# Kernel tuning notes

Hardware: AMD Instinct MI355X
Metric: run time of the kernel (lower is better)

The kernel has to match this reference:

```python
import jax, jax.numpy as jnp
import numpy as np

VOCAB, E, H, HOPS, HEADS = 32000, 128, 256, 3, 4
N, TM, WLEN, TQ = 32, 50, 20, 20


def _gru(x_tbe, h0, Wih, Whh, bih, bhh):
    # x_tbe: [T, B, E] time-major; h0: [B, H]. PyTorch GRU gate order (r, z, n).
    def step(h, xt):
        gi = xt @ Wih.T + bih
        gh = h @ Whh.T + bhh
        ir, iz, inn = jnp.split(gi, 3, axis=-1)
        hr, hz, hn = jnp.split(gh, 3, axis=-1)
        r = jax.nn.sigmoid(ir + hr)
        z = jax.nn.sigmoid(iz + hz)
        n = jnp.tanh(inn + r * hn)
        return (1.0 - z) * n + z * h, None
    h, _ = jax.lax.scan(step, h0, x_tbe)
    return h


def setup_inputs() -> dict:
    key = jax.random.key(0)
    ks = jax.random.split(key, 24)
    f32 = jnp.float32
    emb = jax.random.uniform(ks[0], (VOCAB, E), f32, -3 ** 0.5, 3 ** 0.5)
    emb = emb.at[0].set(0.0)  # padding_idx=0
    s = 0.05
    inp = {
        'stories': jax.random.randint(ks[1], (N, TM, WLEN), 0, VOCAB),
        'questions': jax.random.randint(ks[2], (N, TQ), 0, VOCAB),
        'emb': emb,
        'q_Wih': jax.random.normal(ks[3], (3 * H, E), f32) * s,
        'q_Whh': jax.random.normal(ks[4], (3 * H, H), f32) * s,
        'q_bih': jnp.zeros((3 * H,), f32),
        'q_bhh': jnp.zeros((3 * H,), f32),
        'i_Wih': jax.random.normal(ks[5], (3 * H, E), f32) * s,
        'i_Whh': jax.random.normal(ks[6], (3 * H, H), f32) * s,
        'i_bih': jnp.zeros((3 * H,), f32),
        'i_bhh': jnp.zeros((3 * H,), f32),
        'Wm': jax.random.normal(ks[7], (HOPS, HEADS, H, H), f32) * s,
        'Wo_w': jax.random.normal(ks[8], (HOPS, H, HEADS * H), f32) * s,
        'Wo_b': jnp.full((HOPS, H), 0.01, f32),
        'ft_W1': jax.random.normal(ks[9], (H, H), f32) * s,
        'ft_b1': jnp.full((H,), 0.01, f32),
        'ft_W2': jax.random.normal(ks[10], (H, H), f32) * s,
        'ft_b2': jnp.full((H,), 0.01, f32),
        'g_W1': jax.random.normal(ks[11], (3 * H, 3 * H), f32) * s,
        'g_b1': jnp.full((3 * H,), 0.01, f32),
        'g_W2': jax.random.normal(ks[12], (3 * H, 3 * H), f32) * s,
        'g_b2': jnp.full((3 * H,), 0.01, f32),
        'V_w': jax.random.normal(ks[13], (VOCAB, 3 * H), f32) * s,
    }
    return inp


def reference(stories, questions, emb, q_Wih, q_Whh, q_bih, q_bhh,
              i_Wih, i_Whh, i_bih, i_bhh, Wm, Wo_w, Wo_b,
              ft_W1, ft_b1, ft_W2, ft_b2, g_W1, g_b1, g_W2, g_b2, V_w):
    n, tm, _ = stories.shape
    h = i_Whh.shape[1]
    hops, heads = Wm.shape[0], Wm.shape[1]

    # ---- input module: per-batch-item GRU; hidden state carries across batch items (as in source loop) ----
    story_embs = emb[stories]  # [N, TM, W, E]
    def bstep(hid, se):  # se: [TM, W, E]
        hid2 = _gru(jnp.swapaxes(se, 0, 1), hid, i_Wih, i_Whh, i_bih, i_bhh)
        return hid2, hid2
    _, memory = jax.lax.scan(bstep, jnp.zeros((tm, h), emb.dtype), story_embs)  # [N, TM, H]

    # ---- question module ----
    q_emb = emb[questions]  # [N, TQ, E]
    q = _gru(jnp.swapaxes(q_emb, 0, 1), jnp.zeros((n, h), emb.dtype), q_Wih, q_Whh, q_bih, q_bhh)  # [N, H]

    def ft(x):
        return jax.nn.relu(jax.nn.relu(x @ ft_W1.T + ft_b1) @ ft_W2.T + ft_b2)

    # ---- multi-hop attention controllers ----
    o_k = ft(q)
    buffers = []
    for hp in range(hops):
        proj = jnp.tanh(jnp.einsum('ntd,hed->nhte', memory, Wm[hp]))      # [N,heads,TM,H]
        scores = jax.nn.softmax(jnp.einsum('nhte,ne->nht', proj, o_k), axis=-1)
        rep = jnp.einsum('nht,ntd->nhd', scores, memory)                   # [N,heads,H]
        buf = rep.reshape(n, heads * h) @ Wo_w[hp].T + Wo_b[hp]            # [N,H]
        buffers.append(buf)
        o_k = ft(buf)
    wb = jnp.stack(buffers, axis=1)  # [N, HOPS, H]

    # ---- RM: all-pairs relation MLP (dropout = identity in eval) ----
    npair = hops * hops
    left = jnp.broadcast_to(wb[:, None, :, :], (n, hops, hops, h)).reshape(n, npair, h)
    right = jnp.broadcast_to(wb[:, :, None, :], (n, hops, hops, h)).reshape(n, npair, h)
    qx = jnp.broadcast_to(q[:, None, :], (n, npair, h))
    comb = jnp.concatenate([left, right, qx], axis=-1)                     # [N, HOPS^2, 3H]
    g = jax.nn.relu(jax.nn.relu(comb @ g_W1.T + g_b1) @ g_W2.T + g_b2)
    reasoning = g.sum(axis=1)                                              # [N, 3H]
    return reasoning @ V_w.T                                               # [N, VOCAB]
```

## Files before the change

kernel.cpp:

```cpp
#include <hip/hip_runtime.h>
#include <cmath>

#define VOCABN 32000
#define EE 128
#define HH 256
#define H3 768
#define HOPSN 3
#define HEADSN 4
#define NB 32
#define TMN 50
#define WLENN 20
#define TQN 20
#define NPOS (NB*TMN*WLENN)
#define NQPOS (NB*TQN)

#define OFF_MEM    0
#define OFF_Q      (OFF_MEM + NB*TMN*HH)
#define OFF_OK     (OFF_Q + NB*HH)
#define OFF_WB     (OFF_OK + NB*HH)
#define OFF_REP    (OFF_WB + NB*HOPSN*HH)
#define OFF_REAS   (OFF_REP + NB*HEADSN*HH)
#define OFF_Y1     (OFF_REAS + NB*H3)
#define OFF_PROJ   (OFF_Y1 + NB*9*H3)
#define OFF_EMBP   OFF_PROJ
#define OFF_GI     (OFF_PROJ + NB*12*TMN*HH)

typedef __fp16 h2 __attribute__((ext_vector_type(2)));

__device__ __forceinline__ float sigm(float x) { return 1.f / (1.f + expf(-x)); }

__device__ __forceinline__ unsigned packh2(float x, float y) {
    h2 h = __builtin_amdgcn_cvt_pkrtz(x, y);
    return __builtin_bit_cast(unsigned, h);
}

__device__ __forceinline__ float fdot2u(unsigned a, unsigned b, float c) {
    return __builtin_amdgcn_fdot2(__builtin_bit_cast(h2, a),
                                  __builtin_bit_cast(h2, b), c, false);
}

#define LW(v, base, i8) { const float4 A_ = reinterpret_cast<const float4*>(base)[2*(i8)];     \
                          const float4 B_ = reinterpret_cast<const float4*>(base)[2*(i8)+1];   \
                          v.x = packh2(A_.x, A_.y); v.y = packh2(A_.z, A_.w);                  \
                          v.z = packh2(B_.x, B_.y); v.w = packh2(B_.z, B_.w); }

__global__ __launch_bounds__(256) void k_pack(const float* __restrict__ emb, float* __restrict__ ws)
{
    unsigned* __restrict__ embp = (unsigned*)(ws + OFF_EMBP);
    const int idx = blockIdx.x * 256 + threadIdx.x;
    if (idx < VOCABN * (EE / 2)) {
        const float2 e2 = reinterpret_cast<const float2*>(emb)[idx];
        embp[idx] = packh2(e2.x, e2.y);
    }
}

#define GIB 64
__global__ __launch_bounds__(768) void k_gi2(const int* __restrict__ stories,
                                             const int* __restrict__ questions,
                                             const float* __restrict__ iWih,
                                             const float* __restrict__ qWih,
                                             const float* __restrict__ ibih, const float* __restrict__ ibhh,
                                             const float* __restrict__ qbih, const float* __restrict__ qbhh,
                                             float* __restrict__ ws)
{
    __fp16* __restrict__ gi = (__fp16*)(ws + OFF_GI);
    const unsigned* __restrict__ embp = (const unsigned*)(ws + OFF_EMBP);
    const int j = threadIdx.x;
    const bool isq = blockIdx.x >= (NPOS / GIB);
    const int pblk = isq ? (blockIdx.x - NPOS / GIB) : blockIdx.x;
    const int p0 = pblk * GIB;
    const size_t g0 = (isq ? (size_t)NPOS : 0) + (size_t)p0;
    const int* __restrict__ toks = isq ? (questions + p0) : (stories + p0);
    const float* __restrict__ Wih = isq ? qWih : iWih;
    const float* __restrict__ bih = isq ? qbih : ibih;
    const float* __restrict__ bhh = isq ? qbhh : ibhh;
    const float bias = (j < 2 * HH) ? (bih[j] + bhh[j]) : bih[j];
    const float* wrowp = Wih + (size_t)j * EE;
    uint4 v_0, v_1, v_2, v_3, v_4, v_5, v_6, v_7, v_8, v_9, v_10, v_11, v_12, v_13, v_14, v_15;
    LW(v_0, wrowp, 0)  LW(v_1, wrowp, 1)  LW(v_2, wrowp, 2)  LW(v_3, wrowp, 3)
    LW(v_4, wrowp, 4)  LW(v_5, wrowp, 5)  LW(v_6, wrowp, 6)  LW(v_7, wrowp, 7)
    LW(v_8, wrowp, 8)  LW(v_9, wrowp, 9)  LW(v_10, wrowp, 10) LW(v_11, wrowp, 11)
    LW(v_12, wrowp, 12) LW(v_13, wrowp, 13) LW(v_14, wrowp, 14) LW(v_15, wrowp, 15)

#define DOTG(i) { const uint4 xv = xg[i];                                     \
    acc = fdot2u(xv.x, v_##i.x, acc); acc = fdot2u(xv.y, v_##i.y, acc);       \
    acc = fdot2u(xv.z, v_##i.z, acc); acc = fdot2u(xv.w, v_##i.w, acc); }

    for (int p = 0; p < GIB; ++p) {
        const int tok = toks[p];
        const uint4* __restrict__ xg =
            reinterpret_cast<const uint4*>(embp + (size_t)tok * (EE / 2));
        float acc = bias;
        DOTG(0)  DOTG(1)  DOTG(2)  DOTG(3)  DOTG(4)  DOTG(5)  DOTG(6)  DOTG(7)
        DOTG(8)  DOTG(9)  DOTG(10) DOTG(11) DOTG(12) DOTG(13) DOTG(14) DOTG(15)
        gi[(g0 + p) * H3 + j] = (__fp16)acc;
    }
#undef DOTG
}

__global__ __attribute__((amdgpu_flat_work_group_size(512, 512), amdgpu_waves_per_eu(2, 2)))
void k_gru7(
    const float* __restrict__ iWhh, const float* __restrict__ qWhh,
    const float* __restrict__ ibhh, const float* __restrict__ qbhh,
    float* __restrict__ ws)
{
    __shared__ unsigned hp32[HH / 2];
    __shared__ float red[HH * 5];
    const int tid = threadIdx.x;
    const int j = tid & 255, kh = tid >> 8;
    const int blk = blockIdx.x;
    const bool isq = blk >= TMN;
    const float* __restrict__ Whh = isq ? qWhh : iWhh;
    const float* row0 = Whh + (size_t)j * HH + kh * 128;
    const float* row1 = Whh + (size_t)(HH + j) * HH + kh * 128;
    const float* row2 = Whh + (size_t)(2 * HH + j) * HH + kh * 128;
    uint4 w0_0, w0_1, w0_2, w0_3, w0_4, w0_5, w0_6, w0_7,
          w0_8, w0_9, w0_10, w0_11, w0_12, w0_13, w0_14, w0_15;
    uint4 w1_0, w1_1, w1_2, w1_3, w1_4, w1_5, w1_6, w1_7,
          w1_8, w1_9, w1_10, w1_11, w1_12, w1_13, w1_14, w1_15;
    uint4 w2_0, w2_1, w2_2, w2_3, w2_4, w2_5, w2_6, w2_7,
          w2_8, w2_9, w2_10, w2_11, w2_12, w2_13, w2_14, w2_15;
    LW(w0_0, row0, 0)  LW(w0_1, row0, 1)  LW(w0_2, row0, 2)  LW(w0_3, row0, 3)
    LW(w0_4, row0, 4)  LW(w0_5, row0, 5)  LW(w0_6, row0, 6)  LW(w0_7, row0, 7)
    LW(w0_8, row0, 8)  LW(w0_9, row0, 9)  LW(w0_10, row0, 10) LW(w0_11, row0, 11)
    LW(w0_12, row0, 12) LW(w0_13, row0, 13) LW(w0_14, row0, 14) LW(w0_15, row0, 15)
    LW(w1_0, row1, 0)  LW(w1_1, row1, 1)  LW(w1_2, row1, 2)  LW(w1_3, row1, 3)
    LW(w1_4, row1, 4)  LW(w1_5, row1, 5)  LW(w1_6, row1, 6)  LW(w1_7, row1, 7)
    LW(w1_8, row1, 8)  LW(w1_9, row1, 9)  LW(w1_10, row1, 10) LW(w1_11, row1, 11)
    LW(w1_12, row1, 12) LW(w1_13, row1, 13) LW(w1_14, row1, 14) LW(w1_15, row1, 15)
    LW(w2_0, row2, 0)  LW(w2_1, row2, 1)  LW(w2_2, row2, 2)  LW(w2_3, row2, 3)
    LW(w2_4, row2, 4)  LW(w2_5, row2, 5)  LW(w2_6, row2, 6)  LW(w2_7, row2, 7)
    LW(w2_8, row2, 8)  LW(w2_9, row2, 9)  LW(w2_10, row2, 10) LW(w2_11, row2, 11)
    LW(w2_12, row2, 12) LW(w2_13, row2, 13) LW(w2_14, row2, 14) LW(w2_15, row2, 15)

    float bnH = 0.f, hstate = 0.f;
    if (kh == 0) bnH = (isq ? qbhh : ibhh)[2 * HH + j];
    if (tid < HH / 2) hp32[tid] = 0u;
    const __fp16* __restrict__ gib = (const __fp16*)(ws + OFF_GI)
                                     + (isq ? (size_t)NPOS * H3 : 0);
    float* __restrict__ memv = ws + OFF_MEM;
    float* __restrict__ qv   = ws + OFF_Q;
    __syncthreads();

#define DOT(i) { const uint4 hv = hp4[kh * 16 + (i)];                        \
    a0 = fdot2u(hv.x, w0_##i.x, a0); a0 = fdot2u(hv.y, w0_##i.y, a0);        \
    a0 = fdot2u(hv.z, w0_##i.z, a0); a0 = fdot2u(hv.w, w0_##i.w, a0);        \
    a1 = fdot2u(hv.x, w1_##i.x, a1); a1 = fdot2u(hv.y, w1_##i.y, a1);        \
    a1 = fdot2u(hv.z, w1_##i.z, a1); a1 = fdot2u(hv.w, w1_##i.w, a1);        \
    a2 = fdot2u(hv.x, w2_##i.x, a2); a2 = fdot2u(hv.y, w2_##i.y, a2);        \
    a2 = fdot2u(hv.z, w2_##i.z, a2); a2 = fdot2u(hv.w, w2_##i.w, a2); }

    const int nOuter = isq ? 1 : NB;
    const int c = isq ? (blk - TMN) : blk;
    for (int n = 0; n < nOuter; ++n) {
        for (int t = 0; t < WLENN; ++t) {
            const int pos = isq ? (c * TQN + t) : ((n * TMN + c) * WLENN + t);
            float gir = 0.f, giz = 0.f, gin = 0.f;
            if (kh == 0) {
                const size_t gb = (size_t)pos * H3;
                gir = (float)gib[gb + j];
                giz = (float)gib[gb + HH + j];
                gin = (float)gib[gb + 2 * HH + j];
            }
            float a0 = 0.f, a1 = 0.f, a2 = 0.f;
            const uint4* hp4 = reinterpret_cast<const uint4*>(hp32);
            DOT(0)  DOT(1)  DOT(2)  DOT(3)  DOT(4)  DOT(5)  DOT(6)  DOT(7)
            DOT(8)  DOT(9)  DOT(10) DOT(11) DOT(12) DOT(13) DOT(14) DOT(15)
            if (kh == 1) { red[j * 5 + 0] = a0; red[j * 5 + 1] = a1; red[j * 5 + 2] = a2; }
            __syncthreads();
            if (kh == 0) {
                const float* rr = red + j * 5;
                const float r  = sigm(a0 + rr[0] + gir);
                const float z  = sigm(a1 + rr[1] + giz);
                const float nn = tanhf(gin + r * (a2 + rr[2] + bnH));
                hstate = (1.f - z) * nn + z * hstate;
                reinterpret_cast<__fp16*>(hp32)[j] = (__fp16)hstate;
                if (t == WLENN - 1) {
                    if (isq) qv[c * HH + j] = hstate;
                    else     memv[(size_t)(n * TMN + c) * HH + j] = hstate;
                }
            }
            __syncthreads();
        }
    }
#undef DOT
}

__global__ __launch_bounds__(256) void k_ft(const float* __restrict__ src, float* __restrict__ dst,
                                            const float* __restrict__ W1, const float* __restrict__ b1,
                                            const float* __restrict__ W2, const float* __restrict__ b2)
{
    __shared__ float xr[HH];
    __shared__ float y1[HH];
    const int n = blockIdx.x, j = threadIdx.x;
    xr[j] = src[n * HH + j];
    __syncthreads();
    float acc = b1[j];
    const float4* w1 = reinterpret_cast<const float4*>(W1 + j * HH);
    #pragma unroll 4
    for (int k4 = 0; k4 < HH / 4; ++k4) {
        const float4 w = w1[k4];
        const float4 x = *reinterpret_cast<const float4*>(&xr[k4 * 4]);
        acc = fmaf(x.x, w.x, fmaf(x.y, w.y, fmaf(x.z, w.z, fmaf(x.w, w.w, acc))));
    }
    y1[j] = fmaxf(acc, 0.f);
    __syncthreads();
    acc = b2[j];
    const float4* w2 = reinterpret_cast<const float4*>(W2 + j * HH);
    #pragma unroll 4
    for (int k4 = 0; k4 < HH / 4; ++k4) {
        const float4 w = w2[k4];
        const float4 x = *reinterpret_cast<const float4*>(&y1[k4 * 4]);
        acc = fmaf(x.x, w.x, fmaf(x.y, w.y, fmaf(x.z, w.z, fmaf(x.w, w.w, acc))));
    }
    dst[n * HH + j] = fmaxf(acc, 0.f);
}

__global__ __launch_bounds__(256) void k_proj(const float* __restrict__ Wm, float* __restrict__ ws)
{
    __shared__ float mem_s[TMN][HH];
    const int n = blockIdx.x / 12, he = blockIdx.x % 12;
    const int e = threadIdx.x;
    const float* __restrict__ memory = ws + OFF_MEM + n * TMN * HH;
    for (int idx = e; idx < TMN * HH; idx += HH)
        (&mem_s[0][0])[idx] = memory[idx];
    __syncthreads();
    float p[TMN];
    #pragma unroll
    for (int t = 0; t < TMN; ++t) p[t] = 0.f;
    const float4* wrow = reinterpret_cast<const float4*>(Wm + ((size_t)he * HH + e) * HH);
    for (int d4 = 0; d4 < HH / 4; ++d4) {
        const float4 w = wrow[d4];
        #pragma unroll
        for (int t = 0; t < TMN; ++t) {
            const float4 m = *reinterpret_cast<const float4*>(&mem_s[t][d4 * 4]);
            p[t] = fmaf(m.x, w.x, fmaf(m.y, w.y, fmaf(m.z, w.z, fmaf(m.w, w.w, p[t]))));
        }
    }
    float* __restrict__ proj = ws + OFF_PROJ + ((size_t)(n * 12 + he) * TMN) * HH;
    #pragma unroll
    for (int t = 0; t < TMN; ++t) proj[t * HH + e] = tanhf(p[t]);
}

__global__ __launch_bounds__(256) void k_attn2(float* __restrict__ ws, int hp)
{
    __shared__ float wred[4][TMN];
    __shared__ float sc[TMN];
    const int n = blockIdx.x / HEADSN, hh = blockIdx.x % HEADSN;
    const int e = threadIdx.x;
    const float* __restrict__ proj = ws + OFF_PROJ + ((size_t)(n * 12 + hp * HEADSN + hh) * TMN) * HH;
    const float* __restrict__ memory = ws + OFF_MEM + n * TMN * HH;
    const float okv = (ws + OFF_OK)[n * HH + e];
    const int lane = e & 63, wv = e >> 6;
    #pragma unroll 10
    for (int t = 0; t < TMN; ++t) {
        float v = proj[t * HH + e] * okv;
        #pragma unroll
        for (int off = 32; off > 0; off >>= 1) v += __shfl_xor(v, off);
        if (lane == 0) wred[wv][t] = v;
    }
    __syncthreads();
    if (e < TMN) sc[e] = wred[0][e] + wred[1][e] + wred[2][e] + wred[3][e];
    __syncthreads();
    if (e == 0) {
        float mx = sc[0];
        for (int t = 1; t < TMN; ++t) mx = fmaxf(mx, sc[t]);
        float sum = 0.f;
        for (int t = 0; t < TMN; ++t) { const float ex = expf(sc[t] - mx); sc[t] = ex; sum += ex; }
        const float inv = 1.f / sum;
        for (int t = 0; t < TMN; ++t) sc[t] *= inv;
    }
    __syncthreads();
    float r = 0.f;
    #pragma unroll 10
    for (int t = 0; t < TMN; ++t) r = fmaf(sc[t], memory[t * HH + e], r);
    (ws + OFF_REP)[(n * HEADSN + hh) * HH + e] = r;
}

__global__ __launch_bounds__(256) void k_buf(const float* __restrict__ Wo_w, const float* __restrict__ Wo_b,
                                             const float* __restrict__ W1, const float* __restrict__ b1,
                                             const float* __restrict__ W2, const float* __restrict__ b2,
                                             float* __restrict__ ws, int hp)
{
    __shared__ float repf[HEADSN * HH];
    __shared__ float bufs[HH];
    __shared__ float y1[HH];
    const int n = blockIdx.x, j = threadIdx.x;
    const float* __restrict__ rep = ws + OFF_REP + n * HEADSN * HH;
    for (int idx = j; idx < HEADSN * HH; idx += HH) repf[idx] = rep[idx];
    __syncthreads();
    float acc = Wo_b[hp * HH + j];
    const float4* wrow = reinterpret_cast<const float4*>(Wo_w + ((size_t)hp * HH + j) * (HEADSN * HH));
    #pragma unroll 4
    for (int c4 = 0; c4 < HEADSN * HH / 4; ++c4) {
        const float4 w = wrow[c4];
        const float4 x = *reinterpret_cast<const float4*>(&repf[c4 * 4]);
        acc = fmaf(x.x, w.x, fmaf(x.y, w.y, fmaf(x.z, w.z, fmaf(x.w, w.w, acc))));
    }
    (ws + OFF_WB)[(n * HOPSN + hp) * HH + j] = acc;
    bufs[j] = acc;
    __syncthreads();
    float a1 = b1[j];
    const float4* w1 = reinterpret_cast<const float4*>(W1 + j * HH);
    #pragma unroll 4
    for (int k4 = 0; k4 < HH / 4; ++k4) {
        const float4 w = w1[k4];
        const float4 x = *reinterpret_cast<const float4*>(&bufs[k4 * 4]);
        a1 = fmaf(x.x, w.x, fmaf(x.y, w.y, fmaf(x.z, w.z, fmaf(x.w, w.w, a1))));
    }
    y1[j] = fmaxf(a1, 0.f);
    __syncthreads();
    float a2 = b2[j];
    const float4* w2 = reinterpret_cast<const float4*>(W2 + j * HH);
    #pragma unroll 4
    for (int k4 = 0; k4 < HH / 4; ++k4) {
        const float4 w = w2[k4];
        const float4 x = *reinterpret_cast<const float4*>(&y1[k4 * 4]);
        a2 = fmaf(x.x, w.x, fmaf(x.y, w.y, fmaf(x.z, w.z, fmaf(x.w, w.w, a2))));
    }
    (ws + OFF_OK)[n * HH + j] = fmaxf(a2, 0.f);
}

__global__ __launch_bounds__(256) void k_rm1(const float* __restrict__ gW1, const float* __restrict__ gb1,
                                             float* __restrict__ ws)
{
    __shared__ float comb[9 * H3];
    const int n = blockIdx.x / 3, ot = blockIdx.x % 3;
    const int o = ot * 256 + threadIdx.x;
    const float* __restrict__ wb = ws + OFF_WB + n * HOPSN * HH;
    const float* __restrict__ qv = ws + OFF_Q + n * HH;
    for (int idx = threadIdx.x; idx < 9 * H3; idx += 256) {
        const int p = idx / H3, cc = idx - p * H3;
        const int ii = p / 3, jj = p % 3;
        float v;
        if (cc < HH)           v = wb[jj * HH + cc];
        else if (cc < 2 * HH)  v = wb[ii * HH + (cc - HH)];
        else                   v = qv[cc - 2 * HH];
        comb[idx] = v;
    }
    __syncthreads();
    float acc[9];
    const float b = gb1[o];
    #pragma unroll
    for (int p = 0; p < 9; ++p) acc[p] = b;
    const float4* w1 = reinterpret_cast<const float4*>(gW1 + (size_t)o * H3);
    for (int c4 = 0; c4 < H3 / 4; ++c4) {
        const float4 w = w1[c4];
        #pragma unroll
        for (int p = 0; p < 9; ++p) {
            const float4 x = *reinterpret_cast<const float4*>(&comb[p * H3 + c4 * 4]);
            acc[p] = fmaf(x.x, w.x, fmaf(x.y, w.y, fmaf(x.z, w.z, fmaf(x.w, w.w, acc[p]))));
        }
    }
    float* __restrict__ y1 = ws + OFF_Y1 + (size_t)n * 9 * H3;
    #pragma unroll
    for (int p = 0; p < 9; ++p) y1[p * H3 + o] = fmaxf(acc[p], 0.f);
}

__global__ __launch_bounds__(256) void k_rm2(const float* __restrict__ gW2, const float* __restrict__ gb2,
                                             float* __restrict__ ws)
{
    __shared__ float y1s[9 * H3];
    const int n = blockIdx.x / 3, ot = blockIdx.x % 3;
    const int o = ot * 256 + threadIdx.x;
    const float* __restrict__ y1 = ws + OFF_Y1 + (size_t)n * 9 * H3;
    for (int idx = threadIdx.x; idx < 9 * H3; idx += 256) y1s[idx] = y1[idx];
    __syncthreads();
    float acc[9];
    const float b = gb2[o];
    #pragma unroll
    for (int p = 0; p < 9; ++p) acc[p] = b;
    const float4* w2 = reinterpret_cast<const float4*>(gW2 + (size_t)o * H3);
    for (int c4 = 0; c4 < H3 / 4; ++c4) {
        const float4 w = w2[c4];
        #pragma unroll
        for (int p = 0; p < 9; ++p) {
            const float4 x = *reinterpret_cast<const float4*>(&y1s[p * H3 + c4 * 4]);
            acc[p] = fmaf(x.x, w.x, fmaf(x.y, w.y, fmaf(x.z, w.z, fmaf(x.w, w.w, acc[p]))));
        }
    }
    float s = 0.f;
    #pragma unroll
    for (int p = 0; p < 9; ++p) s += fmaxf(acc[p], 0.f);
    (ws + OFF_REAS)[n * H3 + o] = s;
}

#define RST 36
__global__ __launch_bounds__(256) void k_out(const float* __restrict__ V_w, const float* __restrict__ ws,
                                             float* __restrict__ out)
{
    __shared__ float rsT[H3 * RST];
    const int tid = threadIdx.x;
    const int v = blockIdx.x * 128 + (tid & 127);
    const int nh = tid >> 7;
    for (int idx = tid; idx < NB * H3; idx += 256) {
        const int n = idx / H3, d = idx - n * H3;
        rsT[d * RST + n] = (ws + OFF_REAS)[idx];
    }
    __syncthreads();
    float acc[16];
    #pragma unroll
    for (int i = 0; i < 16; ++i) acc[i] = 0.f;
    const float4* vw = reinterpret_cast<const float4*>(V_w + (size_t)v * H3);
    for (int d4 = 0; d4 < H3 / 4; ++d4) {
        const float4 w = vw[d4];
        #pragma unroll
        for (int dd = 0; dd < 4; ++dd) {
            const float wd = (dd == 0) ? w.x : (dd == 1) ? w.y : (dd == 2) ? w.z : w.w;
            const float* rr = &rsT[(d4 * 4 + dd) * RST + nh * 16];
            #pragma unroll
            for (int q = 0; q < 4; ++q) {
                const float4 r4 = *reinterpret_cast<const float4*>(rr + 4 * q);
                acc[4 * q + 0] = fmaf(wd, r4.x, acc[4 * q + 0]);
                acc[4 * q + 1] = fmaf(wd, r4.y, acc[4 * q + 1]);
                acc[4 * q + 2] = fmaf(wd, r4.z, acc[4 * q + 2]);
                acc[4 * q + 3] = fmaf(wd, r4.w, acc[4 * q + 3]);
            }
        }
    }
    #pragma unroll
    for (int i = 0; i < 16; ++i)
        out[(size_t)(nh * 16 + i) * VOCABN + v] = acc[i];
}

extern "C" void kernel_launch(void* const* d_in, const int* in_sizes, int n_in,
                              void* d_out, int out_size, void* d_ws, size_t ws_size,
                              hipStream_t stream)
{
    const int*   stories   = (const int*)d_in[0];
    const int*   questions = (const int*)d_in[1];
    const float* emb   = (const float*)d_in[2];
    const float* qWih  = (const float*)d_in[3];
    const float* qWhh  = (const float*)d_in[4];
    const float* qbih  = (const float*)d_in[5];
    const float* qbhh  = (const float*)d_in[6];
    const float* iWih  = (const float*)d_in[7];
    const float* iWhh  = (const float*)d_in[8];
    const float* ibih  = (const float*)d_in[9];
    const float* ibhh  = (const float*)d_in[10];
    const float* Wm    = (const float*)d_in[11];
    const float* Wo_w  = (const float*)d_in[12];
    const float* Wo_b  = (const float*)d_in[13];
    const float* ftW1  = (const float*)d_in[14];
    const float* ftb1  = (const float*)d_in[15];
    const float* ftW2  = (const float*)d_in[16];
    const float* ftb2  = (const float*)d_in[17];
    const float* gW1   = (const float*)d_in[18];
    const float* gb1   = (const float*)d_in[19];
    const float* gW2   = (const float*)d_in[20];
    const float* gb2   = (const float*)d_in[21];
    const float* V_w   = (const float*)d_in[22];
    float* ws  = (float*)d_ws;
    float* out = (float*)d_out;

    hipLaunchKernelGGL(k_pack, dim3((VOCABN * (EE / 2) + 255) / 256), dim3(256), 0, stream, emb, ws);
    hipLaunchKernelGGL(k_gi2, dim3((NPOS + NQPOS) / GIB), dim3(H3), 0, stream,
                       stories, questions, iWih, qWih, ibih, ibhh, qbih, qbhh, ws);
    hipLaunchKernelGGL(k_gru7, dim3(TMN + NB), dim3(512), 0, stream,
                       iWhh, qWhh, ibhh, qbhh, ws);
    hipLaunchKernelGGL(k_ft, dim3(NB), dim3(HH), 0, stream, ws + OFF_Q, ws + OFF_OK, ftW1, ftb1, ftW2, ftb2);
    hipLaunchKernelGGL(k_proj, dim3(NB * 12), dim3(256), 0, stream, Wm, ws);
    for (int hp = 0; hp < HOPSN; ++hp) {
        hipLaunchKernelGGL(k_attn2, dim3(NB * HEADSN), dim3(256), 0, stream, ws, hp);
        hipLaunchKernelGGL(k_buf, dim3(NB), dim3(256), 0, stream, Wo_w, Wo_b, ftW1, ftb1, ftW2, ftb2, ws, hp);
    }
    hipLaunchKernelGGL(k_rm1, dim3(NB * 3), dim3(256), 0, stream, gW1, gb1, ws);
    hipLaunchKernelGGL(k_rm2, dim3(NB * 3), dim3(256), 0, stream, gW2, gb2, ws);
    hipLaunchKernelGGL(k_out, dim3(VOCABN / 128), dim3(256), 0, stream, V_w, ws, out);
}
```

Before: 1.481 ms.

## Fuse embedding fp16 packing into GI kernel via shared-memory token staging

Drops the separate pass that converts the whole 32000x128 embedding table to packed fp16. The input-gate kernel now gathers only the 64 token rows each block needs, converts them to fp16 and stages them in shared memory before the dot-product loop. This avoids converting the entire vocabulary, saves a kernel launch, and removes repeated global gathers in the inner loop, at the cost of a block-wide sync. The GRU kernel's shared memory is also padded to about 88KB, apparently to limit how many of its blocks share a compute unit.

```diff
diff --git a/kernel.cpp b/kernel.cpp
--- a/kernel.cpp
+++ b/kernel.cpp
@@ -22,7 +22,6 @@
 #define OFF_REAS   (OFF_REP + NB*HEADSN*HH)
 #define OFF_Y1     (OFF_REAS + NB*H3)
 #define OFF_PROJ   (OFF_Y1 + NB*9*H3)
-#define OFF_EMBP   OFF_PROJ
 #define OFF_GI     (OFF_PROJ + NB*12*TMN*HH)
 
 typedef __fp16 h2 __attribute__((ext_vector_type(2)));
@@ -44,27 +43,18 @@
                           v.x = packh2(A_.x, A_.y); v.y = packh2(A_.z, A_.w);                  \
                           v.z = packh2(B_.x, B_.y); v.w = packh2(B_.z, B_.w); }
 
-__global__ __launch_bounds__(256) void k_pack(const float* __restrict__ emb, float* __restrict__ ws)
-{
-    unsigned* __restrict__ embp = (unsigned*)(ws + OFF_EMBP);
-    const int idx = blockIdx.x * 256 + threadIdx.x;
-    if (idx < VOCABN * (EE / 2)) {
-        const float2 e2 = reinterpret_cast<const float2*>(emb)[idx];
-        embp[idx] = packh2(e2.x, e2.y);
-    }
-}
-
 #define GIB 64
-__global__ __launch_bounds__(768) void k_gi2(const int* __restrict__ stories,
-                                             const int* __restrict__ questions,
-                                             const float* __restrict__ iWih,
-                                             const float* __restrict__ qWih,
-                                             const float* __restrict__ ibih, const float* __restrict__ ibhh,
-                                             const float* __restrict__ qbih, const float* __restrict__ qbhh,
-                                             float* __restrict__ ws)
-{
+__global__ __launch_bounds__(768) void k_gi(const int* __restrict__ stories,
+                                            const int* __restrict__ questions,
+                                            const float* __restrict__ emb,
+                                            const float* __restrict__ iWih,
+                                            const float* __restrict__ qWih,
+                                            const float* __restrict__ ibih, const float* __restrict__ ibhh,
+                                            const float* __restrict__ qbih, const float* __restrict__ qbhh,
+                                            float* __restrict__ ws)
+{
+    __shared__ unsigned xs[GIB][EE / 2];
     __fp16* __restrict__ gi = (__fp16*)(ws + OFF_GI);
-    const unsigned* __restrict__ embp = (const unsigned*)(ws + OFF_EMBP);
     const int j = threadIdx.x;
     const bool isq = blockIdx.x >= (NPOS / GIB);
     const int pblk = isq ? (blockIdx.x - NPOS / GIB) : blockIdx.x;
@@ -82,14 +72,20 @@
     LW(v_8, wrowp, 8)  LW(v_9, wrowp, 9)  LW(v_10, wrowp, 10) LW(v_11, wrowp, 11)
     LW(v_12, wrowp, 12) LW(v_13, wrowp, 13) LW(v_14, wrowp, 14) LW(v_15, wrowp, 15)
 
-#define DOTG(i) { const uint4 xv = xg[i];                                     \
+    for (int idx = j; idx < GIB * (EE / 2); idx += H3) {
+        const int p = idx >> 6, c = idx & 63;
+        const int tok = toks[p];
+        const float2 e2 = reinterpret_cast<const float2*>(emb + (size_t)tok * EE)[c];
+        xs[p][c] = packh2(e2.x, e2.y);
+    }
+    __syncthreads();
+
+#define DOTG(i) { const uint4 xv = x4[i];                                     \
     acc = fdot2u(xv.x, v_##i.x, acc); acc = fdot2u(xv.y, v_##i.y, acc);       \
     acc = fdot2u(xv.z, v_##i.z, acc); acc = fdot2u(xv.w, v_##i.w, acc); }
 
     for (int p = 0; p < GIB; ++p) {
-        const int tok = toks[p];
-        const uint4* __restrict__ xg =
-            reinterpret_cast<const uint4*>(embp + (size_t)tok * (EE / 2));
+        const uint4* x4 = reinterpret_cast<const uint4*>(&xs[p][0]);
         float acc = bias;
         DOTG(0)  DOTG(1)  DOTG(2)  DOTG(3)  DOTG(4)  DOTG(5)  DOTG(6)  DOTG(7)
         DOTG(8)  DOTG(9)  DOTG(10) DOTG(11) DOTG(12) DOTG(13) DOTG(14) DOTG(15)
@@ -98,14 +94,16 @@
 #undef DOTG
 }
 
+#define LDSF 22016
 __global__ __attribute__((amdgpu_flat_work_group_size(512, 512), amdgpu_waves_per_eu(2, 2)))
-void k_gru7(
+void k_gru8(
     const float* __restrict__ iWhh, const float* __restrict__ qWhh,
     const float* __restrict__ ibhh, const float* __restrict__ qbhh,
     float* __restrict__ ws)
 {
-    __shared__ unsigned hp32[HH / 2];
-    __shared__ float red[HH * 5];
+    __shared__ float ldsb[LDSF];
+    unsigned* hp32 = (unsigned*)ldsb;
+    float* red = ldsb + 128;
     const int tid = threadIdx.x;
     const int j = tid & 255, kh = tid >> 8;
     const int blk = blockIdx.x;
@@ -453,10 +451,9 @@
     float* ws  = (float*)d_ws;
     float* out = (float*)d_out;
 
-    hipLaunchKernelGGL(k_pack, dim3((VOCABN * (EE / 2) + 255) / 256), dim3(256), 0, stream, emb, ws);
-    hipLaunchKernelGGL(k_gi2, dim3((NPOS + NQPOS) / GIB), dim3(H3), 0, stream,
-                       stories, questions, iWih, qWih, ibih, ibhh, qbih, qbhh, ws);
-    hipLaunchKernelGGL(k_gru7, dim3(TMN + NB), dim3(512), 0, stream,
+    hipLaunchKernelGGL(k_gi, dim3((NPOS + NQPOS) / GIB), dim3(H3), 0, stream,
+                       stories, questions, emb, iWih, qWih, ibih, ibhh, qbih, qbhh, ws);
+    hipLaunchKernelGGL(k_gru8, dim3(TMN + NB), dim3(512), 0, stream,
                        iWhh, qWhh, ibhh, qbhh, ws);
     hipLaunchKernelGGL(k_ft, dim3(NB), dim3(HH), 0, stream, ws + OFF_Q, ws + OFF_OK, ftW1, ftb1, ftW2, ftb2);
     hipLaunchKernelGGL(k_proj, dim3(NB * 12), dim3(256), 0, stream, Wm, ws);
```

New measurement: 1.361 ms. -8.1%, faster.
